# Kernel tuning notes

Measured on AMD Instinct MI355X. Metric: run time of the kernel, lower is better.

Reference implementation:

```python
import jax, jax.numpy as jnp
import numpy as np
import math

N_HEADS = 4          # h2_dim*n_heads must equal g_dim for the stacked layers
H2_DIM = 32
G_DIM = 128
N_REL = 4
N_LAYERS = 2
PAST_W, FUT_W, PERIODIC = 5, 5, [15]
LN_EPS = 1e-5
BN_EPS = 1e-5


def _build_edges(d):
    ei, et = [], []
    for t in range(d):
        ei.append([t, t]); et.append(0)                      # self-loop
        for off in range(1, PAST_W + 1):
            if t - off >= 0:
                ei.append([t, t - off]); et.append(1)        # past
        for off in range(1, FUT_W + 1):
            if t + off < d:
                ei.append([t, t + off]); et.append(2)        # future
        for off in PERIODIC:
            if t + off < d:
                ei.append([t, t + off]); et.append(3)        # periodic fwd
            if t - off >= 0:
                ei.append([t, t - off]); et.append(3)        # periodic bwd
    return np.array(ei, dtype=np.int64).T, np.array(et, dtype=np.int64)


def setup_inputs() -> dict:
    key = jax.random.key(0)
    b, d, h, w, c = 4, 2048, 8, 8, 192
    ks = jax.random.split(key, 24)
    s = 0.05
    ei, et = _build_edges(d)
    inp = {
        'x': jax.random.normal(ks[0], (b, d, h, w, c), dtype=jnp.float32),
        'edge_index': jnp.asarray(ei),
        'edge_type': jnp.asarray(et),
        'fe_fc_w': jax.random.normal(ks[1], (c, G_DIM), dtype=jnp.float32) * s,
        'fe_fc_b': jnp.zeros((G_DIM,), jnp.float32),
        'fe_ln_g': jnp.ones((G_DIM,), jnp.float32),
        'fe_ln_b': jnp.zeros((G_DIM,), jnp.float32),
        'w_rel': jax.random.normal(ks[2], (N_LAYERS, N_REL, G_DIM, G_DIM), dtype=jnp.float32) * s,
        'w_root': jax.random.normal(ks[3], (N_LAYERS, G_DIM, G_DIM), dtype=jnp.float32) * s,
        'rgcn_b': jnp.zeros((N_LAYERS, G_DIM), jnp.float32),
        'wq': jax.random.normal(ks[4], (N_LAYERS, G_DIM, N_HEADS * H2_DIM), dtype=jnp.float32) * s,
        'bq': jnp.zeros((N_LAYERS, N_HEADS * H2_DIM), jnp.float32),
        'wk': jax.random.normal(ks[5], (N_LAYERS, G_DIM, N_HEADS * H2_DIM), dtype=jnp.float32) * s,
        'bk': jnp.zeros((N_LAYERS, N_HEADS * H2_DIM), jnp.float32),
        'wv': jax.random.normal(ks[6], (N_LAYERS, G_DIM, N_HEADS * H2_DIM), dtype=jnp.float32) * s,
        'bv': jnp.zeros((N_LAYERS, N_HEADS * H2_DIM), jnp.float32),
        'wskip': jax.random.normal(ks[7], (N_LAYERS, G_DIM, N_HEADS * H2_DIM), dtype=jnp.float32) * s,
        'bskip': jnp.zeros((N_LAYERS, N_HEADS * H2_DIM), jnp.float32),
        'bn_g': jnp.ones((N_LAYERS, N_HEADS * H2_DIM), jnp.float32),
        'bn_b': jnp.zeros((N_LAYERS, N_HEADS * H2_DIM), jnp.float32),
    }
    return inp


def _forward(x, edge_index, edge_type, fe_fc_w, fe_fc_b, fe_ln_g, fe_ln_b,
             w_rel, w_root, rgcn_b, wq, bq, wk, bk, wv, bv, wskip, bskip, bn_g, bn_b):
    d = x.shape[1]
    src, dst = edge_index[0], edge_index[1]
    rel_masks = [(edge_type == r).astype(jnp.float32) for r in range(N_REL)]
    inv_sqrt_c = 1.0 / math.sqrt(H2_DIM)

    def graph_fwd(xi):  # xi: [d,h,w,c]
        feat = xi.mean(axis=(1, 2))                         # adaptive avg pool -> [d,c]
        hfe = feat @ fe_fc_w + fe_fc_b                      # [d,g]
        mu = hfe.mean(-1, keepdims=True)
        var = ((hfe - mu) ** 2).mean(-1, keepdims=True)
        nf = (hfe - mu) / jnp.sqrt(var + LN_EPS) * fe_ln_g + fe_ln_b

        for l in range(N_LAYERS):
            # ---- RGCNConv (mean aggregation per relation + root) ----
            out = nf @ w_root[l] + rgcn_b[l]
            for r in range(N_REL):
                m = rel_masks[r]
                xr = nf @ w_rel[l, r]                       # [d,g]
                msg = xr[src] * m[:, None]                  # [E,g]
                s = jax.ops.segment_sum(msg, dst, num_segments=d)
                cnt = jax.ops.segment_sum(m, dst, num_segments=d)
                out = out + s / jnp.maximum(cnt, 1.0)[:, None]
            nf1 = out
            # ---- TransformerConv (per-head edge attention) ----
            q = (nf1 @ wq[l] + bq[l]).reshape(d, N_HEADS, H2_DIM)
            k = (nf1 @ wk[l] + bk[l]).reshape(d, N_HEADS, H2_DIM)
            v = (nf1 @ wv[l] + bv[l]).reshape(d, N_HEADS, H2_DIM)
            logits = (q[dst] * k[src]).sum(-1) * inv_sqrt_c  # [E,H]
            mx = jax.ops.segment_max(logits, dst, num_segments=d)
            a = jnp.exp(logits - mx[dst])
            denom = jax.ops.segment_sum(a, dst, num_segments=d)
            alpha = a / denom[dst]                           # softmax over incoming edges
            agg = jax.ops.segment_sum(alpha[:, :, None] * v[src], dst, num_segments=d)
            out2 = agg.reshape(d, N_HEADS * H2_DIM) + nf1 @ wskip[l] + bskip[l]
            # ---- BatchNorm1d (training-mode batch stats over nodes) ----
            bmu = out2.mean(0)
            bvar = ((out2 - bmu) ** 2).mean(0)
            out2 = (out2 - bmu) / jnp.sqrt(bvar + BN_EPS) * bn_g[l] + bn_b[l]
            nf = jax.nn.leaky_relu(out2, 0.01)
        return nf

    return jax.vmap(graph_fwd)(x)                           # [b,d,g]


def reference(x, edge_index, edge_type, fe_fc_w, fe_fc_b, fe_ln_g, fe_ln_b,
              w_rel, w_root, rgcn_b, wq, bq, wk, bk, wv, bv, wskip, bskip, bn_g, bn_b):
    return _forward(x, edge_index, edge_type, fe_fc_w, fe_fc_b, fe_ln_g, fe_ln_b,
                    w_rel, w_root, rgcn_b, wq, bq, wk, bk, wv, bv, wskip, bskip, bn_g, bn_b)
```

## Files before the change

kernel.cpp:

```cpp
#include <hip/hip_runtime.h>
#include <hip/hip_bf16.h>

#define B_ 4
#define D_ 2048
#define HWS 64
#define C_ 192
#define G_ 128
#define NODES (B_*D_)
#define R_ 16
#define HALO_ROWS 48

typedef short bf8_t  __attribute__((ext_vector_type(8)));
typedef float f32x4_t __attribute__((ext_vector_type(4)));
typedef unsigned short us4_t __attribute__((ext_vector_type(4)));

__device__ inline unsigned short f2bf(float f) {
    unsigned int u = __builtin_bit_cast(unsigned int, f);
    unsigned int r = (u + 0x7fffu + ((u >> 16) & 1u)) >> 16;
    return (unsigned short)r;
}
__device__ inline float bf2f(unsigned short h) {
    unsigned int u = ((unsigned int)h) << 16;
    return __builtin_bit_cast(float, u);
}

struct WconvArgs {
    const float* src[16];
    const float* add[16];
};
__global__ __launch_bounds__(256) void wconv_kernel(WconvArgs a, unsigned short* __restrict__ dst)
{
    int m = blockIdx.y;
    int idx = blockIdx.x * 256 + threadIdx.x;
    int n = idx >> 7;
    int k = idx & 127;
    float v = a.src[m][k * G_ + n];
    if (a.add[m]) v += a.add[m][k * G_ + n];
    dst[(size_t)m * 16384 + idx] = f2bf(v);
}

__global__ __launch_bounds__(192) void pool_fc_ln_kernel(
    const float* __restrict__ x, const float* __restrict__ W,
    const float* __restrict__ bias, const float* __restrict__ gam,
    const float* __restrict__ bet, unsigned short* __restrict__ nf)
{
    int u = blockIdx.x;
    int tid = threadIdx.x;
    __shared__ float feat[C_];
    __shared__ float4 red4[4][48];
    __shared__ float red[4];
    __shared__ float stats[2];

    const float4* xb4 = (const float4*)(x + (size_t)u * (HWS * C_));
    int cg = tid % 48;
    int rg = tid / 48;
    float4 a = make_float4(0.f, 0.f, 0.f, 0.f);
    #pragma unroll
    for (int s = 0; s < HWS; s += 4) {
        float4 v = xb4[(size_t)(s + rg) * 48 + cg];
        a.x += v.x; a.y += v.y; a.z += v.z; a.w += v.w;
    }
    red4[rg][cg] = a;
    __syncthreads();
    if (rg == 0) {
        float4 b0 = red4[0][cg], b1 = red4[1][cg], b2 = red4[2][cg], b3 = red4[3][cg];
        feat[cg * 4 + 0] = (b0.x + b1.x + b2.x + b3.x) * (1.0f / HWS);
        feat[cg * 4 + 1] = (b0.y + b1.y + b2.y + b3.y) * (1.0f / HWS);
        feat[cg * 4 + 2] = (b0.z + b1.z + b2.z + b3.z) * (1.0f / HWS);
        feat[cg * 4 + 3] = (b0.w + b1.w + b2.w + b3.w) * (1.0f / HWS);
    }
    __syncthreads();

    float h = 0.f;
    if (tid < G_) {
        h = bias[tid];
        #pragma unroll 4
        for (int c = 0; c < C_; ++c) h += feat[c] * W[c * G_ + tid];
    }
    float s1 = (tid < G_) ? h : 0.f;
    float s2 = (tid < G_) ? h * h : 0.f;
    #pragma unroll
    for (int off = 32; off >= 1; off >>= 1) {
        s1 += __shfl_xor(s1, off, 64);
        s2 += __shfl_xor(s2, off, 64);
    }
    int wid = tid >> 6;
    if ((tid & 63) == 0 && wid < 2) { red[wid] = s1; red[2 + wid] = s2; }
    __syncthreads();
    if (tid == 0) {
        float S = red[0] + red[1];
        float SS = red[2] + red[3];
        float mu = S / G_;
        float var = SS / G_ - mu * mu;
        stats[0] = mu;
        stats[1] = 1.0f / sqrtf(var + 1e-5f);
    }
    __syncthreads();
    if (tid < G_) {
        float v = (h - stats[0]) * stats[1] * gam[tid] + bet[tid];
        nf[(size_t)u * G_ + tid] = f2bf(v);
    }
}

template <bool BNIN>
__global__ __launch_bounds__(256) void rgcn_fused_kernel(
    const unsigned short* __restrict__ nf, const float* __restrict__ xin,
    const float* __restrict__ partials, const float* __restrict__ gam,
    const float* __restrict__ bet,
    const unsigned short* __restrict__ wt,
    const float* __restrict__ rb,
    unsigned short* __restrict__ out)
{
    __shared__ char raw[HALO_ROWS * 256];
    __shared__ char agg[R_ * 1024];
    __shared__ float smu[G_], sivg[G_], sbet[G_];
    __shared__ float sred[2][G_], ssred[2][G_];
    int blk = blockIdx.x;
    int b = blk >> 7;
    int t0 = (blk & 127) * R_;
    int tid = threadIdx.x;

    if constexpr (BNIN) {
        int halfk = tid >> 7;
        int c = tid & 127;
        float s = 0.f, ss = 0.f;
        const float* P = partials + (size_t)b * 128 * 256;
        #pragma unroll 4
        for (int k = halfk * 64; k < halfk * 64 + 64; ++k) {
            s += P[k * 256 + c];
            ss += P[k * 256 + G_ + c];
        }
        sred[halfk][c] = s;
        ssred[halfk][c] = ss;
        __syncthreads();
        if (tid < G_) {
            float S = sred[0][tid] + sred[1][tid];
            float SS = ssred[0][tid] + ssred[1][tid];
            float mu = S / D_;
            float var = SS / D_ - mu * mu;
            float inv = 1.0f / sqrtf(var + 1e-5f);
            smu[tid] = mu;
            sivg[tid] = inv * gam[tid];
            sbet[tid] = bet[tid];
        }
        __syncthreads();
        const float* xb = xin + (size_t)b * D_ * G_;
        #pragma unroll
        for (int p = 0; p < 3; ++p) {
            int task = tid + p * 256;
            int i = task >> 4, c16 = task & 15;
            int t = t0 - 15 + i;
            bf8_t v8 = {0, 0, 0, 0, 0, 0, 0, 0};
            if (t >= 0 && t < D_) {
                const float* vp = xb + (size_t)t * G_ + c16 * 8;
                #pragma unroll
                for (int e = 0; e < 8; ++e) {
                    int c = c16 * 8 + e;
                    float y = (vp[e] - smu[c]) * sivg[c] + sbet[c];
                    y = (y > 0.f) ? y : 0.01f * y;
                    v8[e] = (short)f2bf(y);
                }
            }
            *(bf8_t*)(raw + ((i * 256 + c16 * 16) ^ ((i & 7) << 4))) = v8;
        }
    } else {
        const unsigned short* src = nf + (size_t)b * D_ * G_;
        #pragma unroll
        for (int p = 0; p < 3; ++p) {
            int task = tid + p * 256;
            int i = task >> 4, c16 = task & 15;
            int t = t0 - 15 + i;
            bf8_t v = {0, 0, 0, 0, 0, 0, 0, 0};
            if (t >= 0 && t < D_) v = *(const bf8_t*)(src + (size_t)t * G_ + c16 * 8);
            *(bf8_t*)(raw + ((i * 256 + c16 * 16) ^ ((i & 7) << 4))) = v;
        }
    }
    __syncthreads();

    #pragma unroll
    for (int p = 0; p < 4; ++p) {
        int task = tid + p * 256;
        int c16 = task & 15, rel = (task >> 4) & 3, row = task >> 6;
        int t = t0 + row;
        int ctr = row + 15;
        float s[8] = {0.f,0.f,0.f,0.f,0.f,0.f,0.f,0.f};
        float scale = 1.f;
        if (rel == 0) {
            bf8_t v = *(const bf8_t*)(raw + ((ctr * 256 + c16 * 16) ^ ((ctr & 7) << 4)));
            #pragma unroll
            for (int e = 0; e < 8; ++e) s[e] = bf2f((unsigned short)v[e]);
        } else if (rel == 1) {
            #pragma unroll
            for (int o = 1; o <= 5; ++o) if (t + o < D_) {
                int i = ctr + o;
                bf8_t v = *(const bf8_t*)(raw + ((i * 256 + c16 * 16) ^ ((i & 7) << 4)));
                #pragma unroll
                for (int e = 0; e < 8; ++e) s[e] += bf2f((unsigned short)v[e]);
            }
            scale = 1.f / (float)max(min(5, D_ - 1 - t), 1);
        } else if (rel == 2) {
            #pragma unroll
            for (int o = 1; o <= 5; ++o) if (t - o >= 0) {
                int i = ctr - o;
                bf8_t v = *(const bf8_t*)(raw + ((i * 256 + c16 * 16) ^ ((i & 7) << 4)));
                #pragma unroll
                for (int e = 0; e < 8; ++e) s[e] += bf2f((unsigned short)v[e]);
            }
            scale = 1.f / (float)max(min(5, t), 1);
        } else {
            int cnt = 0;
            if (t >= 15) {
                int i = ctr - 15;
                bf8_t v = *(const bf8_t*)(raw + ((i * 256 + c16 * 16) ^ ((i & 7) << 4)));
                #pragma unroll
                for (int e = 0; e < 8; ++e) s[e] += bf2f((unsigned short)v[e]);
                cnt++;
            }
            if (t + 15 < D_) {
                int i = ctr + 15;
                bf8_t v = *(const bf8_t*)(raw + ((i * 256 + c16 * 16) ^ ((i & 7) << 4)));
                #pragma unroll
                for (int e = 0; e < 8; ++e) s[e] += bf2f((unsigned short)v[e]);
                cnt++;
            }
            scale = 1.f / (float)max(cnt, 1);
        }
        bf8_t o8;
        #pragma unroll
        for (int e = 0; e < 8; ++e) o8[e] = (short)f2bf(s[e] * scale);
        *(bf8_t*)(agg + ((row * 1024 + rel * 256 + c16 * 16) ^ ((row & 7) << 4))) = o8;
    }
    __syncthreads();

    int l = tid & 63, wv = tid >> 6;
    int l15 = l & 15, kgrp = l >> 4;
    int col16 = blockIdx.y * 4 + wv;
    f32x4_t acc = (f32x4_t){0.f, 0.f, 0.f, 0.f};

    for (int ks = 0; ks < 16; ++ks) {
        int rel = ks >> 2, kk = ks & 3;
        bf8_t a = *(const bf8_t*)(agg +
            ((l15 * 1024 + rel * 256 + kk * 64 + kgrp * 16) ^ ((l15 & 7) << 4)));
        bf8_t bf = *(const bf8_t*)(wt + rel * 16384 +
            (size_t)(col16 * 16 + l15) * G_ + kk * 32 + kgrp * 8);
        acc = __builtin_amdgcn_mfma_f32_16x16x32_bf16(a, bf, acc, 0, 0, 0);
    }

    unsigned short* outb = out + (size_t)b * D_ * G_;
    int rbase = t0 + kgrp * 4;
    int col = col16 * 16 + l15;
    float rbv = rb[col];
    #pragma unroll
    for (int j = 0; j < 4; ++j)
        outb[(size_t)(rbase + j) * G_ + col] = f2bf(acc[j] + rbv);
}

__device__ inline void stage_halo48(const unsigned short* __restrict__ src,
                                    int t0, char* raw, int tid)
{
    #pragma unroll
    for (int p = 0; p < 3; ++p) {
        int task = tid + p * 256;
        int i = task >> 4, c16 = task & 15;
        int t = t0 - 15 + i;
        bf8_t v = {0, 0, 0, 0, 0, 0, 0, 0};
        if (t >= 0 && t < D_) v = *(const bf8_t*)(src + (size_t)t * G_ + c16 * 8);
        *(bf8_t*)(raw + ((i * 256 + c16 * 16) ^ ((i & 7) << 4))) = v;
    }
}

__global__ __launch_bounds__(256) void qkvs_attn_kernel(
    const unsigned short* __restrict__ nf1,
    const unsigned short* __restrict__ wt,
    const float* __restrict__ bq, const float* __restrict__ bk,
    const float* __restrict__ bv, const float* __restrict__ bsk,
    float* __restrict__ out2, float* __restrict__ partials)
{
    __shared__ char raw[HALO_ROWS * 256];
    __shared__ unsigned short kls[HALO_ROWS * 64];
    __shared__ unsigned short vls[HALO_ROWS * 64];
    __shared__ unsigned short qls[R_ * 64];
    __shared__ float sls[R_ * 64];
    int blk = blockIdx.x, tid = threadIdx.x;
    int b = blk >> 7, t0 = (blk & 127) * R_;
    int y = blockIdx.y;

    stage_halo48(nf1 + (size_t)b * D_ * G_, t0, raw, tid);
    __syncthreads();

    int l = tid & 63, wvid = tid >> 6;
    int l15 = l & 15, kgrp = l >> 4;
    #pragma unroll
    for (int i = 0; i < 2; ++i) {
        int job = wvid + i * 4;
        int m, frag;
        if (job < 3)      { m = 1; frag = job; }
        else if (job < 6) { m = 2; frag = job - 3; }
        else if (job == 6){ m = 0; frag = 0; }
        else              { m = 3; frag = 0; }
        bool halo = (m == 1) | (m == 2);
        int rawrow = halo ? (frag * 16 + l15) : (15 + l15);
        const unsigned short* wm = wt + (size_t)m * 16384;
        const float* bias = (m == 0) ? bq : (m == 1) ? bk : (m == 2) ? bv : bsk;

        bf8_t a[4];
        #pragma unroll
        for (int kc = 0; kc < 4; ++kc)
            a[kc] = *(const bf8_t*)(raw +
                ((rawrow * 256 + kc * 64 + kgrp * 16) ^ ((rawrow & 7) << 4)));
        f32x4_t acc[4];
        #pragma unroll
        for (int n = 0; n < 4; ++n) acc[n] = (f32x4_t){0.f, 0.f, 0.f, 0.f};
        #pragma unroll
        for (int kc = 0; kc < 4; ++kc) {
            #pragma unroll
            for (int n = 0; n < 4; ++n) {
                int col = y * 64 + n * 16 + l15;
                bf8_t bf = *(const bf8_t*)(wm +
                    (size_t)col * G_ + kc * 32 + kgrp * 8);
                acc[n] = __builtin_amdgcn_mfma_f32_16x16x32_bf16(a[kc], bf, acc[n], 0, 0, 0);
            }
        }
        int r0 = frag * 16 + kgrp * 4;
        #pragma unroll
        for (int n = 0; n < 4; ++n) {
            int ln = n * 16 + l15;
            float bb = bias[y * 64 + ln];
            #pragma unroll
            for (int j = 0; j < 4; ++j) {
                float v = acc[n][j] + bb;
                int rr = r0 + j;
                if (m == 1)      kls[rr * 64 + ln] = f2bf(v);
                else if (m == 2) vls[rr * 64 + ln] = f2bf(v);
                else if (m == 0) qls[rr * 64 + ln] = f2bf(v);
                else             sls[rr * 64 + ln] = v;
            }
        }
    }
    __syncthreads();

    int j = tid & 63, quarter = tid >> 6;
    const float invs = 0.17677669529663687f;
    float ps = 0.f, pss = 0.f;
    float* o2b = out2 + (size_t)b * D_ * G_;
    const int offs[13] = {0, 1, 2, 3, 4, 5, -1, -2, -3, -4, -5, -15, 15};
    for (int it = 0; it < 4; ++it) {
        int tl = it * 4 + quarter;
        int t = t0 + tl;
        float q = bf2f(qls[tl * 64 + j]);
        float lg[13], vv[13];
        #pragma unroll
        for (int n = 0; n < 13; ++n) {
            int ts = t + offs[n];
            bool ok = (ts >= 0) && (ts < D_);
            int ki = tl + 15 + offs[n];
            float kk = ok ? bf2f(kls[ki * 64 + j]) : 0.f;
            vv[n] = ok ? bf2f(vls[ki * 64 + j]) : 0.f;
            float p = q * kk;
            p += __shfl_xor(p, 16, 32);
            p += __shfl_xor(p, 8, 32);
            p += __shfl_xor(p, 4, 32);
            p += __shfl_xor(p, 2, 32);
            p += __shfl_xor(p, 1, 32);
            lg[n] = ok ? p * invs : -1e30f;
        }
        float m = lg[0];
        #pragma unroll
        for (int n = 1; n < 13; ++n) m = fmaxf(m, lg[n]);
        float den = 0.f, aggv = 0.f;
        #pragma unroll
        for (int n = 0; n < 13; ++n) {
            float e = expf(lg[n] - m);
            den += e;
            aggv += e * vv[n];
        }
        float o = aggv / den + sls[tl * 64 + j];
        o2b[(size_t)t * G_ + y * 64 + j] = o;
        ps += o; pss += o * o;
    }

    __syncthreads();
    float* red = (float*)raw;
    red[quarter * 64 + j] = ps;
    red[256 + quarter * 64 + j] = pss;
    __syncthreads();
    if (tid < 64) {
        float s = 0.f, ss = 0.f;
        #pragma unroll
        for (int qq = 0; qq < 4; ++qq) {
            s += red[qq * 64 + tid];
            ss += red[256 + qq * 64 + tid];
        }
        float* P = partials + ((size_t)b * 128 + (blk & 127)) * 256;
        P[y * 64 + tid] = s;
        P[128 + y * 64 + tid] = ss;
    }
}

__global__ __launch_bounds__(256) void bn_apply_kernel(
    const float* __restrict__ X, const float* __restrict__ partials,
    const float* __restrict__ gam, const float* __restrict__ bet,
    float* __restrict__ out)
{
    int chunk = blockIdx.x;
    int b = blockIdx.y;
    int tid = threadIdx.x;
    __shared__ float smu[G_], sinv[G_];
    if (tid < G_) {
        float s = 0.f, ss = 0.f;
        const float* P = partials + (size_t)b * 128 * 256;
        #pragma unroll 4
        for (int k = 0; k < 128; ++k) {
            s += P[k * 256 + tid];
            ss += P[k * 256 + G_ + tid];
        }
        float mu = s / D_;
        float var = ss / D_ - mu * mu;
        smu[tid] = mu;
        sinv[tid] = 1.0f / sqrtf(var + 1e-5f);
    }
    __syncthreads();

    const float4* base4 = (const float4*)(X + ((size_t)b * D_ + chunk * 64) * G_);
    int c4 = (tid & 31) * 4;
    float m0 = smu[c4], m1 = smu[c4 + 1], m2 = smu[c4 + 2], m3 = smu[c4 + 3];
    float i0 = sinv[c4] * gam[c4],     i1 = sinv[c4 + 1] * gam[c4 + 1];
    float i2 = sinv[c4 + 2] * gam[c4 + 2], i3 = sinv[c4 + 3] * gam[c4 + 3];
    float b0 = bet[c4], b1 = bet[c4 + 1], b2 = bet[c4 + 2], b3 = bet[c4 + 3];
    #pragma unroll
    for (int p = 0; p < 8; ++p) {
        float4 v = base4[p * 256 + tid];
        float4 y;
        y.x = (v.x - m0) * i0 + b0;
        y.y = (v.y - m1) * i1 + b1;
        y.z = (v.z - m2) * i2 + b2;
        y.w = (v.w - m3) * i3 + b3;
        y.x = (y.x > 0.f) ? y.x : 0.01f * y.x;
        y.y = (y.y > 0.f) ? y.y : 0.01f * y.y;
        y.z = (y.z > 0.f) ? y.z : 0.01f * y.z;
        y.w = (y.w > 0.f) ? y.w : 0.01f * y.w;
        float4* ob = (float4*)(out + ((size_t)b * D_ + chunk * 64) * G_);
        ob[p * 256 + tid] = y;
    }
}

extern "C" void kernel_launch(void* const* d_in, const int* in_sizes, int n_in,
                              void* d_out, int out_size, void* d_ws, size_t ws_size,
                              hipStream_t stream)
{
    (void)in_sizes; (void)n_in; (void)out_size; (void)ws_size;
    const float* x      = (const float*)d_in[0];
    const float* fe_w   = (const float*)d_in[3];
    const float* fe_b   = (const float*)d_in[4];
    const float* ln_g   = (const float*)d_in[5];
    const float* ln_b   = (const float*)d_in[6];
    const float* w_rel  = (const float*)d_in[7];
    const float* w_root = (const float*)d_in[8];
    const float* rgcn_b = (const float*)d_in[9];
    const float* wq  = (const float*)d_in[10];
    const float* bq  = (const float*)d_in[11];
    const float* wk  = (const float*)d_in[12];
    const float* bk  = (const float*)d_in[13];
    const float* wv  = (const float*)d_in[14];
    const float* bv  = (const float*)d_in[15];
    const float* wsk = (const float*)d_in[16];
    const float* bsk = (const float*)d_in[17];
    const float* bn_g = (const float*)d_in[18];
    const float* bn_b = (const float*)d_in[19];

    float* ws   = (float*)d_ws;
    float* out2 = ws;
    float* partials = out2 + (size_t)NODES * G_;
    unsigned short* nf_bf  = (unsigned short*)(partials + 4 * 128 * 256);
    unsigned short* nf1_bf = nf_bf + (size_t)NODES * G_;
    unsigned short* wbf    = nf1_bf + (size_t)NODES * G_;

    WconvArgs wa;
    for (int l = 0; l < 2; ++l) {
        for (int r = 0; r < 4; ++r) {
            wa.src[l * 8 + r] = w_rel + ((size_t)l * 4 + r) * G_ * G_;
            wa.add[l * 8 + r] = (r == 0) ? (w_root + (size_t)l * G_ * G_) : nullptr;
        }
        wa.src[l * 8 + 4] = wq  + (size_t)l * G_ * G_; wa.add[l * 8 + 4] = nullptr;
        wa.src[l * 8 + 5] = wk  + (size_t)l * G_ * G_; wa.add[l * 8 + 5] = nullptr;
        wa.src[l * 8 + 6] = wv  + (size_t)l * G_ * G_; wa.add[l * 8 + 6] = nullptr;
        wa.src[l * 8 + 7] = wsk + (size_t)l * G_ * G_; wa.add[l * 8 + 7] = nullptr;
    }
    wconv_kernel<<<dim3(64, 16), 256, 0, stream>>>(wa, wbf);

    pool_fc_ln_kernel<<<NODES, 192, 0, stream>>>(x, fe_w, fe_b, ln_g, ln_b, nf_bf);

    rgcn_fused_kernel<false><<<dim3(512, 2), 256, 0, stream>>>(
        nf_bf, nullptr, nullptr, nullptr, nullptr,
        wbf, rgcn_b, nf1_bf);
    qkvs_attn_kernel<<<dim3(512, 2), 256, 0, stream>>>(
        nf1_bf, wbf + (size_t)4 * 16384,
        bq, bk, bv, bsk, out2, partials);

    rgcn_fused_kernel<true><<<dim3(512, 2), 256, 0, stream>>>(
        nullptr, out2, partials, bn_g, bn_b,
        wbf + (size_t)8 * 16384, rgcn_b + G_, nf1_bf);
    qkvs_attn_kernel<<<dim3(512, 2), 256, 0, stream>>>(
        nf1_bf, wbf + (size_t)12 * 16384,
        bq + G_, bk + G_, bv + G_, bsk + G_, out2, partials);

    bn_apply_kernel<<<dim3(32, 4), 256, 0, stream>>>(
        out2, partials, bn_g + G_, bn_b + G_, (float*)d_out);
}
```

Measured before the change: 225.6 us.

## Fuse RGCN and attention into one per-layer kernel with recomputed halo

Merges the RGCN aggregation+GEMM kernel and the QKV/attention kernel into a single layer kernel per graph layer. Each block stages a wider 78-row input halo, recomputes the RGCN output for 48 rows (including the attention halo) in shared memory, then runs the QKV projections and windowed attention from it. This removes the nf1 global round-trip and two launches per layer. In exchange it does about three times the RGCN work per block and halves the grid (512 blocks instead of 1024), with larger shared memory use lowering occupancy. Output and partial buffers are double-buffered across layers.

```diff
diff --git a/kernel.cpp b/kernel.cpp
--- a/kernel.cpp
+++ b/kernel.cpp
@@ -8,11 +8,11 @@
 #define G_ 128
 #define NODES (B_*D_)
 #define R_ 16
-#define HALO_ROWS 48
+#define NF1R 48
+#define RAWR 78
 
 typedef short bf8_t  __attribute__((ext_vector_type(8)));
 typedef float f32x4_t __attribute__((ext_vector_type(4)));
-typedef unsigned short us4_t __attribute__((ext_vector_type(4)));
 
 __device__ inline unsigned short f2bf(float f) {
     unsigned int u = __builtin_bit_cast(unsigned int, f);
@@ -102,298 +102,299 @@
     }
 }
 
+struct ShQOut {
+    unsigned short kls[NF1R * 64];
+    unsigned short vls[NF1R * 64];
+    unsigned short qls[R_ * 64];
+    float sls[R_ * 64];
+    float redsc[512];
+};
+struct ShBN {
+    float smu[G_], sivg[G_], sbet[G_];
+    float sred[2][G_], ssred[2][G_];
+};
+struct ShL {
+    char raw[RAWR * 256];
+    char nf1e[NF1R * 256];
+    union {
+        char agg[R_ * 1024];
+        ShQOut q;
+        ShBN bn;
+    } u;
+};
+
 template <bool BNIN>
-__global__ __launch_bounds__(256) void rgcn_fused_kernel(
-    const unsigned short* __restrict__ nf, const float* __restrict__ xin,
-    const float* __restrict__ partials, const float* __restrict__ gam,
-    const float* __restrict__ bet,
+__global__ __launch_bounds__(256) void layer_kernel(
+    const unsigned short* __restrict__ nfin,
+    const float* __restrict__ xin,
+    const float* __restrict__ partials_in,
+    const float* __restrict__ gam, const float* __restrict__ bet,
     const unsigned short* __restrict__ wt,
     const float* __restrict__ rb,
-    unsigned short* __restrict__ out)
+    const float* __restrict__ bq, const float* __restrict__ bk,
+    const float* __restrict__ bv, const float* __restrict__ bsk,
+    float* __restrict__ out2, float* __restrict__ partials_out)
 {
-    __shared__ char raw[HALO_ROWS * 256];
-    __shared__ char agg[R_ * 1024];
-    __shared__ float smu[G_], sivg[G_], sbet[G_];
-    __shared__ float sred[2][G_], ssred[2][G_];
+    __shared__ ShL sh;
     int blk = blockIdx.x;
+    int tid = threadIdx.x;
     int b = blk >> 7;
     int t0 = (blk & 127) * R_;
-    int tid = threadIdx.x;
 
     if constexpr (BNIN) {
-        int halfk = tid >> 7;
-        int c = tid & 127;
-        float s = 0.f, ss = 0.f;
-        const float* P = partials + (size_t)b * 128 * 256;
-        #pragma unroll 4
-        for (int k = halfk * 64; k < halfk * 64 + 64; ++k) {
-            s += P[k * 256 + c];
-            ss += P[k * 256 + G_ + c];
-        }
-        sred[halfk][c] = s;
-        ssred[halfk][c] = ss;
+        {
+            int halfk = tid >> 7;
+            int c = tid & 127;
+            float s = 0.f, ss = 0.f;
+            const float* P = partials_in + (size_t)b * 128 * 256;
+            #pragma unroll 4
+            for (int k = halfk * 64; k < halfk * 64 + 64; ++k) {
+                s += P[k * 256 + c];
+                ss += P[k * 256 + G_ + c];
+            }
+            sh.u.bn.sred[halfk][c] = s;
+            sh.u.bn.ssred[halfk][c] = ss;
+        }
         __syncthreads();
         if (tid < G_) {
-            float S = sred[0][tid] + sred[1][tid];
-            float SS = ssred[0][tid] + ssred[1][tid];
+            float S = sh.u.bn.sred[0][tid] + sh.u.bn.sred[1][tid];
+            float SS = sh.u.bn.ssred[0][tid] + sh.u.bn.ssred[1][tid];
             float mu = S / D_;
             float var = SS / D_ - mu * mu;
             float inv = 1.0f / sqrtf(var + 1e-5f);
-            smu[tid] = mu;
-            sivg[tid] = inv * gam[tid];
-            sbet[tid] = bet[tid];
+            sh.u.bn.smu[tid] = mu;
+            sh.u.bn.sivg[tid] = inv * gam[tid];
+            sh.u.bn.sbet[tid] = bet[tid];
         }
         __syncthreads();
         const float* xb = xin + (size_t)b * D_ * G_;
         #pragma unroll
-        for (int p = 0; p < 3; ++p) {
+        for (int p = 0; p < 5; ++p) {
             int task = tid + p * 256;
-            int i = task >> 4, c16 = task & 15;
-            int t = t0 - 15 + i;
-            bf8_t v8 = {0, 0, 0, 0, 0, 0, 0, 0};
-            if (t >= 0 && t < D_) {
-                const float* vp = xb + (size_t)t * G_ + c16 * 8;
-                #pragma unroll
-                for (int e = 0; e < 8; ++e) {
-                    int c = c16 * 8 + e;
-                    float y = (vp[e] - smu[c]) * sivg[c] + sbet[c];
-                    y = (y > 0.f) ? y : 0.01f * y;
-                    v8[e] = (short)f2bf(y);
-                }
-            }
-            *(bf8_t*)(raw + ((i * 256 + c16 * 16) ^ ((i & 7) << 4))) = v8;
+            if (task < RAWR * 16) {
+                int i = task >> 4, c16 = task & 15;
+                int t = t0 - 30 + i;
+                bf8_t v8 = {0, 0, 0, 0, 0, 0, 0, 0};
+                if (t >= 0 && t < D_) {
+                    const float* vp = xb + (size_t)t * G_ + c16 * 8;
+                    #pragma unroll
+                    for (int e = 0; e < 8; ++e) {
+                        int c = c16 * 8 + e;
+                        float yv = (vp[e] - sh.u.bn.smu[c]) * sh.u.bn.sivg[c] + sh.u.bn.sbet[c];
+                        yv = (yv > 0.f) ? yv : 0.01f * yv;
+                        v8[e] = (short)f2bf(yv);
+                    }
+                }
+                *(bf8_t*)(sh.raw + ((i * 256 + c16 * 16) ^ ((i & 7) << 4))) = v8;
+            }
         }
     } else {
-        const unsigned short* src = nf + (size_t)b * D_ * G_;
+        const unsigned short* src = nfin + (size_t)b * D_ * G_;
         #pragma unroll
-        for (int p = 0; p < 3; ++p) {
+        for (int p = 0; p < 5; ++p) {
             int task = tid + p * 256;
-            int i = task >> 4, c16 = task & 15;
-            int t = t0 - 15 + i;
-            bf8_t v = {0, 0, 0, 0, 0, 0, 0, 0};
-            if (t >= 0 && t < D_) v = *(const bf8_t*)(src + (size_t)t * G_ + c16 * 8);
-            *(bf8_t*)(raw + ((i * 256 + c16 * 16) ^ ((i & 7) << 4))) = v;
-        }
-    }
-    __syncthreads();
-
-    #pragma unroll
-    for (int p = 0; p < 4; ++p) {
-        int task = tid + p * 256;
-        int c16 = task & 15, rel = (task >> 4) & 3, row = task >> 6;
-        int t = t0 + row;
-        int ctr = row + 15;
-        float s[8] = {0.f,0.f,0.f,0.f,0.f,0.f,0.f,0.f};
-        float scale = 1.f;
-        if (rel == 0) {
-            bf8_t v = *(const bf8_t*)(raw + ((ctr * 256 + c16 * 16) ^ ((ctr & 7) << 4)));
-            #pragma unroll
-            for (int e = 0; e < 8; ++e) s[e] = bf2f((unsigned short)v[e]);
-        } else if (rel == 1) {
-            #pragma unroll
-            for (int o = 1; o <= 5; ++o) if (t + o < D_) {
-                int i = ctr + o;
-                bf8_t v = *(const bf8_t*)(raw + ((i * 256 + c16 * 16) ^ ((i & 7) << 4)));
-                #pragma unroll
-                for (int e = 0; e < 8; ++e) s[e] += bf2f((unsigned short)v[e]);
-            }
-            scale = 1.f / (float)max(min(5, D_ - 1 - t), 1);
-        } else if (rel == 2) {
-            #pragma unroll
-            for (int o = 1; o <= 5; ++o) if (t - o >= 0) {
-                int i = ctr - o;
-                bf8_t v = *(const bf8_t*)(raw + ((i * 256 + c16 * 16) ^ ((i & 7) << 4)));
-                #pragma unroll
-                for (int e = 0; e < 8; ++e) s[e] += bf2f((unsigned short)v[e]);
-            }
-            scale = 1.f / (float)max(min(5, t), 1);
-        } else {
-            int cnt = 0;
-            if (t >= 15) {
-                int i = ctr - 15;
-                bf8_t v = *(const bf8_t*)(raw + ((i * 256 + c16 * 16) ^ ((i & 7) << 4)));
-                #pragma unroll
-                for (int e = 0; e < 8; ++e) s[e] += bf2f((unsigned short)v[e]);
-                cnt++;
-            }
-            if (t + 15 < D_) {
-                int i = ctr + 15;
-                bf8_t v = *(const bf8_t*)(raw + ((i * 256 + c16 * 16) ^ ((i & 7) << 4)));
-                #pragma unroll
-                for (int e = 0; e < 8; ++e) s[e] += bf2f((unsigned short)v[e]);
-                cnt++;
-            }
-            scale = 1.f / (float)max(cnt, 1);
-        }
-        bf8_t o8;
-        #pragma unroll
-        for (int e = 0; e < 8; ++e) o8[e] = (short)f2bf(s[e] * scale);
-        *(bf8_t*)(agg + ((row * 1024 + rel * 256 + c16 * 16) ^ ((row & 7) << 4))) = o8;
+            if (task < RAWR * 16) {
+                int i = task >> 4, c16 = task & 15;
+                int t = t0 - 30 + i;
+                bf8_t v = {0, 0, 0, 0, 0, 0, 0, 0};
+                if (t >= 0 && t < D_) v = *(const bf8_t*)(src + (size_t)t * G_ + c16 * 8);
+                *(bf8_t*)(sh.raw + ((i * 256 + c16 * 16) ^ ((i & 7) << 4))) = v;
+            }
+        }
     }
     __syncthreads();
 
     int l = tid & 63, wv = tid >> 6;
     int l15 = l & 15, kgrp = l >> 4;
-    int col16 = blockIdx.y * 4 + wv;
-    f32x4_t acc = (f32x4_t){0.f, 0.f, 0.f, 0.f};
-
-    for (int ks = 0; ks < 16; ++ks) {
-        int rel = ks >> 2, kk = ks & 3;
-        bf8_t a = *(const bf8_t*)(agg +
-            ((l15 * 1024 + rel * 256 + kk * 64 + kgrp * 16) ^ ((l15 & 7) << 4)));
-        bf8_t bf = *(const bf8_t*)(wt + rel * 16384 +
-            (size_t)(col16 * 16 + l15) * G_ + kk * 32 + kgrp * 8);
-        acc = __builtin_amdgcn_mfma_f32_16x16x32_bf16(a, bf, acc, 0, 0, 0);
-    }
-
-    unsigned short* outb = out + (size_t)b * D_ * G_;
-    int rbase = t0 + kgrp * 4;
-    int col = col16 * 16 + l15;
-    float rbv = rb[col];
-    #pragma unroll
-    for (int j = 0; j < 4; ++j)
-        outb[(size_t)(rbase + j) * G_ + col] = f2bf(acc[j] + rbv);
-}
-
-__device__ inline void stage_halo48(const unsigned short* __restrict__ src,
-                                    int t0, char* raw, int tid)
-{
-    #pragma unroll
-    for (int p = 0; p < 3; ++p) {
-        int task = tid + p * 256;
-        int i = task >> 4, c16 = task & 15;
-        int t = t0 - 15 + i;
-        bf8_t v = {0, 0, 0, 0, 0, 0, 0, 0};
-        if (t >= 0 && t < D_) v = *(const bf8_t*)(src + (size_t)t * G_ + c16 * 8);
-        *(bf8_t*)(raw + ((i * 256 + c16 * 16) ^ ((i & 7) << 4))) = v;
-    }
-}
-
-__global__ __launch_bounds__(256) void qkvs_attn_kernel(
-    const unsigned short* __restrict__ nf1,
-    const unsigned short* __restrict__ wt,
-    const float* __restrict__ bq, const float* __restrict__ bk,
-    const float* __restrict__ bv, const float* __restrict__ bsk,
-    float* __restrict__ out2, float* __restrict__ partials)
-{
-    __shared__ char raw[HALO_ROWS * 256];
-    __shared__ unsigned short kls[HALO_ROWS * 64];
-    __shared__ unsigned short vls[HALO_ROWS * 64];
-    __shared__ unsigned short qls[R_ * 64];
-    __shared__ float sls[R_ * 64];
-    int blk = blockIdx.x, tid = threadIdx.x;
-    int b = blk >> 7, t0 = (blk & 127) * R_;
-    int y = blockIdx.y;
-
-    stage_halo48(nf1 + (size_t)b * D_ * G_, t0, raw, tid);
-    __syncthreads();
-
-    int l = tid & 63, wvid = tid >> 6;
-    int l15 = l & 15, kgrp = l >> 4;
-    #pragma unroll
-    for (int i = 0; i < 2; ++i) {
-        int job = wvid + i * 4;
-        int m, frag;
-        if (job < 3)      { m = 1; frag = job; }
-        else if (job < 6) { m = 2; frag = job - 3; }
-        else if (job == 6){ m = 0; frag = 0; }
-        else              { m = 3; frag = 0; }
-        bool halo = (m == 1) | (m == 2);
-        int rawrow = halo ? (frag * 16 + l15) : (15 + l15);
-        const unsigned short* wm = wt + (size_t)m * 16384;
-        const float* bias = (m == 0) ? bq : (m == 1) ? bk : (m == 2) ? bv : bsk;
-
-        bf8_t a[4];
+
+    for (int ps = 0; ps < 3; ++ps) {
         #pragma unroll
-        for (int kc = 0; kc < 4; ++kc)
-            a[kc] = *(const bf8_t*)(raw +
-                ((rawrow * 256 + kc * 64 + kgrp * 16) ^ ((rawrow & 7) << 4)));
-        f32x4_t acc[4];
+        for (int p = 0; p < 4; ++p) {
+            int task = tid + p * 256;
+            int c16 = task & 15, rel = (task >> 4) & 3, row = task >> 6;
+            int pr = ps * 16 + row;
+            int t = t0 - 15 + pr;
+            int ctr = pr + 15;
+            float s[8] = {0.f,0.f,0.f,0.f,0.f,0.f,0.f,0.f};
+            float scale = 1.f;
+            if (rel == 0) {
+                bf8_t v = *(const bf8_t*)(sh.raw + ((ctr * 256 + c16 * 16) ^ ((ctr & 7) << 4)));
+                #pragma unroll
+                for (int e = 0; e < 8; ++e) s[e] = bf2f((unsigned short)v[e]);
+            } else if (rel == 1) {
+                #pragma unroll
+                for (int o = 1; o <= 5; ++o) if (t + o < D_ && t + o >= 0) {
+                    int i = ctr + o;
+                    bf8_t v = *(const bf8_t*)(sh.raw + ((i * 256 + c16 * 16) ^ ((i & 7) << 4)));
+                    #pragma unroll
+                    for (int e = 0; e < 8; ++e) s[e] += bf2f((unsigned short)v[e]);
+                }
+                scale = 1.f / (float)max(min(5, D_ - 1 - t), 1);
+            } else if (rel == 2) {
+                #pragma unroll
+                for (int o = 1; o <= 5; ++o) if (t - o >= 0 && t - o < D_) {
+                    int i = ctr - o;
+                    bf8_t v = *(const bf8_t*)(sh.raw + ((i * 256 + c16 * 16) ^ ((i & 7) << 4)));
+                    #pragma unroll
+                    for (int e = 0; e < 8; ++e) s[e] += bf2f((unsigned short)v[e]);
+                }
+                scale = 1.f / (float)max(min(5, t), 1);
+            } else {
+                int cnt = 0;
+                if (t >= 15 && t < D_ + 15) {
+                    int i = ctr - 15;
+                    bf8_t v = *(const bf8_t*)(sh.raw + ((i * 256 + c16 * 16) ^ ((i & 7) << 4)));
+                    #pragma unroll
+                    for (int e = 0; e < 8; ++e) s[e] += bf2f((unsigned short)v[e]);
+                    cnt++;
+                }
+                if (t + 15 < D_ && t + 15 >= 0) {
+                    int i = ctr + 15;
+                    bf8_t v = *(const bf8_t*)(sh.raw + ((i * 256 + c16 * 16) ^ ((i & 7) << 4)));
+                    #pragma unroll
+                    for (int e = 0; e < 8; ++e) s[e] += bf2f((unsigned short)v[e]);
+                    cnt++;
+                }
+                scale = 1.f / (float)max(cnt, 1);
+            }
+            bf8_t o8;
+            #pragma unroll
+            for (int e = 0; e < 8; ++e) o8[e] = (short)f2bf(s[e] * scale);
+            *(bf8_t*)(sh.u.agg + ((row * 1024 + rel * 256 + c16 * 16) ^ ((row & 7) << 4))) = o8;
+        }
+        __syncthreads();
+
         #pragma unroll
-        for (int n = 0; n < 4; ++n) acc[n] = (f32x4_t){0.f, 0.f, 0.f, 0.f};
+        for (int y = 0; y < 2; ++y) {
+            int col16 = y * 4 + wv;
+            f32x4_t acc = (f32x4_t){0.f, 0.f, 0.f, 0.f};
+            for (int ks = 0; ks < 16; ++ks) {
+                int rel = ks >> 2, kk = ks & 3;
+                bf8_t a = *(const bf8_t*)(sh.u.agg +
+                    ((l15 * 1024 + rel * 256 + kk * 64 + kgrp * 16) ^ ((l15 & 7) << 4)));
+                bf8_t bf = *(const bf8_t*)(wt + rel * 16384 +
+                    (size_t)(col16 * 16 + l15) * G_ + kk * 32 + kgrp * 8);
+                acc = __builtin_amdgcn_mfma_f32_16x16x32_bf16(a, bf, acc, 0, 0, 0);
+            }
+            int col = col16 * 16 + l15;
+            float rbv = rb[col];
+            #pragma unroll
+            for (int j = 0; j < 4; ++j) {
+                int row = ps * 16 + kgrp * 4 + j;
+                *(unsigned short*)(sh.nf1e +
+                    ((row * 256 + col * 2) ^ ((row & 7) << 4))) = f2bf(acc[j] + rbv);
+            }
+        }
+        __syncthreads();
+    }
+
+    const float invs = 0.17677669529663687f;
+    const int offs[13] = {0, 1, 2, 3, 4, 5, -1, -2, -3, -4, -5, -15, 15};
+    float* o2b = out2 + (size_t)b * D_ * G_;
+
+    for (int y = 0; y < 2; ++y) {
         #pragma unroll
-        for (int kc = 0; kc < 4; ++kc) {
+        for (int i = 0; i < 2; ++i) {
+            int job = wv + i * 4;
+            int m, frag;
+            if (job < 3)      { m = 1; frag = job; }
+            else if (job < 6) { m = 2; frag = job - 3; }
+            else if (job == 6){ m = 0; frag = 0; }
+            else              { m = 3; frag = 0; }
+            bool halo = (m == 1) | (m == 2);
+            int nrow = halo ? (frag * 16 + l15) : (15 + l15);
+            const unsigned short* wm = wt + (size_t)(4 + m) * 16384;
+            const float* bias = (m == 0) ? bq : (m == 1) ? bk : (m == 2) ? bv : bsk;
+
+            bf8_t a[4];
+            #pragma unroll
+            for (int kc = 0; kc < 4; ++kc)
+                a[kc] = *(const bf8_t*)(sh.nf1e +
+                    ((nrow * 256 + kc * 64 + kgrp * 16) ^ ((nrow & 7) << 4)));
+            f32x4_t acc[4];
+            #pragma unroll
+            for (int n = 0; n < 4; ++n) acc[n] = (f32x4_t){0.f, 0.f, 0.f, 0.f};
+            #pragma unroll
+            for (int kc = 0; kc < 4; ++kc) {
+                #pragma unroll
+                for (int n = 0; n < 4; ++n) {
+                    int col = y * 64 + n * 16 + l15;
+                    bf8_t bf = *(const bf8_t*)(wm +
+                        (size_t)col * G_ + kc * 32 + kgrp * 8);
+                    acc[n] = __builtin_amdgcn_mfma_f32_16x16x32_bf16(a[kc], bf, acc[n], 0, 0, 0);
+                }
+            }
+            int r0 = frag * 16 + kgrp * 4;
             #pragma unroll
             for (int n = 0; n < 4; ++n) {
-                int col = y * 64 + n * 16 + l15;
-                bf8_t bf = *(const bf8_t*)(wm +
-                    (size_t)col * G_ + kc * 32 + kgrp * 8);
-                acc[n] = __builtin_amdgcn_mfma_f32_16x16x32_bf16(a[kc], bf, acc[n], 0, 0, 0);
-            }
-        }
-        int r0 = frag * 16 + kgrp * 4;
-        #pragma unroll
-        for (int n = 0; n < 4; ++n) {
-            int ln = n * 16 + l15;
-            float bb = bias[y * 64 + ln];
-            #pragma unroll
-            for (int j = 0; j < 4; ++j) {
-                float v = acc[n][j] + bb;
-                int rr = r0 + j;
-                if (m == 1)      kls[rr * 64 + ln] = f2bf(v);
-                else if (m == 2) vls[rr * 64 + ln] = f2bf(v);
-                else if (m == 0) qls[rr * 64 + ln] = f2bf(v);
-                else             sls[rr * 64 + ln] = v;
-            }
-        }
-    }
-    __syncthreads();
-
-    int j = tid & 63, quarter = tid >> 6;
-    const float invs = 0.17677669529663687f;
-    float ps = 0.f, pss = 0.f;
-    float* o2b = out2 + (size_t)b * D_ * G_;
-    const int offs[13] = {0, 1, 2, 3, 4, 5, -1, -2, -3, -4, -5, -15, 15};
-    for (int it = 0; it < 4; ++it) {
-        int tl = it * 4 + quarter;
-        int t = t0 + tl;
-        float q = bf2f(qls[tl * 64 + j]);
-        float lg[13], vv[13];
-        #pragma unroll
-        for (int n = 0; n < 13; ++n) {
-            int ts = t + offs[n];
-            bool ok = (ts >= 0) && (ts < D_);
-            int ki = tl + 15 + offs[n];
-            float kk = ok ? bf2f(kls[ki * 64 + j]) : 0.f;
-            vv[n] = ok ? bf2f(vls[ki * 64 + j]) : 0.f;
-            float p = q * kk;
-            p += __shfl_xor(p, 16, 32);
-            p += __shfl_xor(p, 8, 32);
-            p += __shfl_xor(p, 4, 32);
-            p += __shfl_xor(p, 2, 32);
-            p += __shfl_xor(p, 1, 32);
-            lg[n] = ok ? p * invs : -1e30f;
-        }
-        float m = lg[0];
-        #pragma unroll
-        for (int n = 1; n < 13; ++n) m = fmaxf(m, lg[n]);
-        float den = 0.f, aggv = 0.f;
-        #pragma unroll
-        for (int n = 0; n < 13; ++n) {
-            float e = expf(lg[n] - m);
-            den += e;
-            aggv += e * vv[n];
-        }
-        float o = aggv / den + sls[tl * 64 + j];
-        o2b[(size_t)t * G_ + y * 64 + j] = o;
-        ps += o; pss += o * o;
-    }
-
-    __syncthreads();
-    float* red = (float*)raw;
-    red[quarter * 64 + j] = ps;
-    red[256 + quarter * 64 + j] = pss;
-    __syncthreads();
-    if (tid < 64) {
-        float s = 0.f, ss = 0.f;
-        #pragma unroll
-        for (int qq = 0; qq < 4; ++qq) {
-            s += red[qq * 64 + tid];
-            ss += red[256 + qq * 64 + tid];
-        }
-        float* P = partials + ((size_t)b * 128 + (blk & 127)) * 256;
-        P[y * 64 + tid] = s;
-        P[128 + y * 64 + tid] = ss;
+                int ln = n * 16 + l15;
+                float bb = bias[y * 64 + ln];
+                #pragma unroll
+                for (int j = 0; j < 4; ++j) {
+                    float v = acc[n][j] + bb;
+                    int rr = r0 + j;
+                    if (m == 1)      sh.u.q.kls[rr * 64 + ln] = f2bf(v);
+                    else if (m == 2) sh.u.q.vls[rr * 64 + ln] = f2bf(v);
+                    else if (m == 0) sh.u.q.qls[rr * 64 + ln] = f2bf(v);
+                    else             sh.u.q.sls[rr * 64 + ln] = v;
+                }
+            }
+        }
+        __syncthreads();
+
+        int j = tid & 63, quarter = tid >> 6;
+        float ps2 = 0.f, pss = 0.f;
+        for (int it = 0; it < 4; ++it) {
+            int tl = it * 4 + quarter;
+            int t = t0 + tl;
+            float q = bf2f(sh.u.q.qls[tl * 64 + j]);
+            float lg[13], vv[13];
+            #pragma unroll
+            for (int n = 0; n < 13; ++n) {
+                int ts = t + offs[n];
+                bool ok = (ts >= 0) && (ts < D_);
+                int ki = tl + 15 + offs[n];
+                float kk = ok ? bf2f(sh.u.q.kls[ki * 64 + j]) : 0.f;
+                vv[n] = ok ? bf2f(sh.u.q.vls[ki * 64 + j]) : 0.f;
+                float p = q * kk;
+                p += __shfl_xor(p, 16, 32);
+                p += __shfl_xor(p, 8, 32);
+                p += __shfl_xor(p, 4, 32);
+                p += __shfl_xor(p, 2, 32);
+                p += __shfl_xor(p, 1, 32);
+                lg[n] = ok ? p * invs : -1e30f;
+            }
+            float m = lg[0];
+            #pragma unroll
+            for (int n = 1; n < 13; ++n) m = fmaxf(m, lg[n]);
+            float den = 0.f, aggv = 0.f;
+            #pragma unroll
+            for (int n = 0; n < 13; ++n) {
+                float e = expf(lg[n] - m);
+                den += e;
+                aggv += e * vv[n];
+            }
+            float o = aggv / den + sh.u.q.sls[tl * 64 + j];
+            o2b[(size_t)t * G_ + y * 64 + j] = o;
+            ps2 += o; pss += o * o;
+        }
+        __syncthreads();
+
+        sh.u.q.redsc[quarter * 64 + j] = ps2;
+        sh.u.q.redsc[256 + quarter * 64 + j] = pss;
+        __syncthreads();
+        if (tid < 64) {
+            float s = 0.f, ss = 0.f;
+            #pragma unroll
+            for (int qq = 0; qq < 4; ++qq) {
+                s += sh.u.q.redsc[qq * 64 + tid];
+                ss += sh.u.q.redsc[256 + qq * 64 + tid];
+            }
+            float* P = partials_out + ((size_t)b * 128 + (blk & 127)) * 256;
+            P[y * 64 + tid] = s;
+            P[128 + y * 64 + tid] = ss;
+        }
+        __syncthreads();
     }
 }
 
@@ -469,11 +470,12 @@
     const float* bn_b = (const float*)d_in[19];
 
     float* ws   = (float*)d_ws;
-    float* out2 = ws;
-    float* partials = out2 + (size_t)NODES * G_;
-    unsigned short* nf_bf  = (unsigned short*)(partials + 4 * 128 * 256);
-    unsigned short* nf1_bf = nf_bf + (size_t)NODES * G_;
-    unsigned short* wbf    = nf1_bf + (size_t)NODES * G_;
+    float* out2a = ws;
+    float* out2b = out2a + (size_t)NODES * G_;
+    float* partialsA = out2b + (size_t)NODES * G_;
+    float* partialsB = partialsA + 4 * 128 * 256;
+    unsigned short* nf_bf = (unsigned short*)(partialsB + 4 * 128 * 256);
+    unsigned short* wbf   = nf_bf + (size_t)NODES * G_;
 
     WconvArgs wa;
     for (int l = 0; l < 2; ++l) {
@@ -490,20 +492,16 @@
 
     pool_fc_ln_kernel<<<NODES, 192, 0, stream>>>(x, fe_w, fe_b, ln_g, ln_b, nf_bf);
 
-    rgcn_fused_kernel<false><<<dim3(512, 2), 256, 0, stream>>>(
+    layer_kernel<false><<<512, 256, 0, stream>>>(
         nf_bf, nullptr, nullptr, nullptr, nullptr,
-        wbf, rgcn_b, nf1_bf);
-    qkvs_attn_kernel<<<dim3(512, 2), 256, 0, stream>>>(
-        nf1_bf, wbf + (size_t)4 * 16384,
-        bq, bk, bv, bsk, out2, partials);
-
-    rgcn_fused_kernel<true><<<dim3(512, 2), 256, 0, stream>>>(
-        nullptr, out2, partials, bn_g, bn_b,
-        wbf + (size_t)8 * 16384, rgcn_b + G_, nf1_bf);
-    qkvs_attn_kernel<<<dim3(512, 2), 256, 0, stream>>>(
-        nf1_bf, wbf + (size_t)12 * 16384,
-        bq + G_, bk + G_, bv + G_, bsk + G_, out2, partials);
+        wbf, rgcn_b,
+        bq, bk, bv, bsk, out2a, partialsA);
+
+    layer_kernel<true><<<512, 256, 0, stream>>>(
+        nullptr, out2a, partialsA, bn_g, bn_b,
+        wbf + (size_t)8 * 16384, rgcn_b + G_,
+        bq + G_, bk + G_, bv + G_, bsk + G_, out2b, partialsB);
 
     bn_apply_kernel<<<dim3(32, 4), 256, 0, stream>>>(
-        out2, partials, bn_g + G_, bn_b + G_, (float*)d_out);
-}
+        out2b, partialsB, bn_g + G_, bn_b + G_, (float*)d_out);
+}
```

After: 298.0 us. 32.1% more time.
